# Optimization experiments

Hardware: AMD Instinct MI355X
Metric: run time of the kernel (lower is better)

## Reference

```python
import jax, jax.numpy as jnp
import numpy as np
import math

B, C, N = 8, 512, 2048

def setup_inputs() -> dict:
    key = jax.random.key(0)
    ks = jax.random.split(key, 7)
    s = 0.02
    return {
        "x": jax.random.normal(ks[0], (B, C, N), dtype=jnp.float32),
        "Wq": jax.random.normal(ks[1], (C // 2, C), dtype=jnp.float32) * s,
        "bq": jax.random.normal(ks[2], (C // 2,), dtype=jnp.float32) * s,
        "Wk": jax.random.normal(ks[3], (C // 2, C), dtype=jnp.float32) * s,
        "bk": jax.random.normal(ks[4], (C // 2,), dtype=jnp.float32) * s,
        "Wv": jax.random.normal(ks[5], (C, C), dtype=jnp.float32) * s,
        "bv": jax.random.normal(ks[6], (C,), dtype=jnp.float32) * s,
    }

def reference(x, Wq, bq, Wk, bk, Wv, bv):
    # pointwise conv1d == channel matmul: (O,C) x (B,C,N) -> (B,O,N)
    Q = jnp.einsum('oc,bcn->bon', Wq, x) + bq[None, :, None]  # (B, C/2, N)
    K = jnp.einsum('oc,bcn->bon', Wk, x) + bk[None, :, None]  # (B, C/2, N)
    V = jnp.einsum('oc,bcn->bon', Wv, x) + bv[None, :, None]  # (B, C, N)
    scale = 1.0 / math.sqrt(K.shape[1])
    A = jnp.einsum('bcn,bcm->bnm', Q, K) * scale              # (B, N, N)
    A = jax.nn.softmax(A, axis=-1)
    out = jnp.einsum('bcm,bnm->bcn', V, A)                    # V @ A^T
    return x + out
```

## Files before the change

### kernel.cpp

```cpp
#include <hip/hip_runtime.h>

#define B_ 8
#define C_ 512
#define N_ 2048
#define O_ 256

typedef unsigned short u16;
typedef unsigned char u8;
typedef unsigned int uint;
typedef float f32x4 __attribute__((ext_vector_type(4)));
typedef int i32x8 __attribute__((ext_vector_type(8)));

#define AS1 __attribute__((address_space(1)))
#define AS3 __attribute__((address_space(3)))

__device__ __forceinline__ u16 f2bf(float f) {
  union { float f; unsigned u; } v; v.f = f;
  return (u16)((v.u + 0x7fffu + ((v.u >> 16) & 1u)) >> 16);
}
__device__ __forceinline__ float bf2f(u16 h) {
  union { uint u; float f; } v; v.u = ((uint)h) << 16; return v.f;
}
__device__ __forceinline__ uint pk4_e4m3(float a, float b, float c, float d) {
  int r = __builtin_amdgcn_cvt_pk_fp8_f32(a, b, 0, false);
  r = __builtin_amdgcn_cvt_pk_fp8_f32(c, d, r, true);
  return (uint)r;
}

union MxFrag { i32x8 v; uint4 q[2]; };

__device__ __forceinline__ void mx_mainloop(
    const u8* __restrict__ Ag, int lda,
    const u8* __restrict__ Bg, int ldb, int K,
    u8 (&As)[128][128], u8 (&Bs)[128][128], f32x4 (&acc)[4][4])
{
  const int t = threadIdx.x;
  const int lane = t & 63;
  const int w = t >> 6;
  const int wm = (w >> 1) * 64, wn = (w & 1) * 64;
  const int lrow = lane & 15, quad = lane >> 4;
  const int swz = lrow & 7;
  const int r8 = lane >> 3;
  const int gsrc = (lane & 7) ^ r8;

  for (int k0 = 0; k0 < K; k0 += 128) {
#pragma unroll
    for (int i = 0; i < 4; i++) {
      int row = i * 32 + w * 8;
      __builtin_amdgcn_global_load_lds(
          (const AS1 uint*)(Ag + (size_t)(row + r8) * lda + k0 + gsrc * 16),
          (AS3 uint*)(&As[row][0]), 16, 0, 0);
      __builtin_amdgcn_global_load_lds(
          (const AS1 uint*)(Bg + (size_t)(row + r8) * ldb + k0 + gsrc * 16),
          (AS3 uint*)(&Bs[row][0]), 16, 0, 0);
    }
    __syncthreads();
    const int g0 = (quad * 2) ^ swz, g1 = (quad * 2 + 1) ^ swz;
    MxFrag af[4], bfr[4];
#pragma unroll
    for (int i = 0; i < 4; i++) {
      const u8* rp = &As[wm + i * 16 + lrow][0];
      af[i].q[0] = *(const uint4*)(rp + g0 * 16);
      af[i].q[1] = *(const uint4*)(rp + g1 * 16);
    }
#pragma unroll
    for (int j = 0; j < 4; j++) {
      const u8* rp = &Bs[wn + j * 16 + lrow][0];
      bfr[j].q[0] = *(const uint4*)(rp + g0 * 16);
      bfr[j].q[1] = *(const uint4*)(rp + g1 * 16);
    }
#pragma unroll
    for (int i = 0; i < 4; i++)
#pragma unroll
      for (int j = 0; j < 4; j++)
        acc[i][j] = __builtin_amdgcn_mfma_scale_f32_16x16x128_f8f6f4(
            af[i].v, bfr[j].v, acc[i][j],
            0, 0,
            0, 0x7f7f7f7f,
            0, 0x7f7f7f7f);
    __syncthreads();
  }
}

__device__ __forceinline__ void mx_mainloop_512(
    const u8* __restrict__ Ag, int lda,
    const u8* __restrict__ Bg, int ldb, int K,
    u8 (&As)[256][128], u8 (&Bs)[128][128], f32x4 (&acc)[4][4])
{
  const int t = threadIdx.x;
  const int lane = t & 63;
  const int w = t >> 6;
  const int wm = (w & 3) * 64, wn = (w >> 2) * 64;
  const int lrow = lane & 15, quad = lane >> 4;
  const int swz = lrow & 7;
  const int r8 = lane >> 3;
  const int gsrc = (lane & 7) ^ r8;

  for (int k0 = 0; k0 < K; k0 += 128) {
#pragma unroll
    for (int s = 0; s < 4; s++) {
      int row = (w * 4 + s) * 8;
      __builtin_amdgcn_global_load_lds(
          (const AS1 uint*)(Ag + (size_t)(row + r8) * lda + k0 + gsrc * 16),
          (AS3 uint*)(&As[row][0]), 16, 0, 0);
    }
#pragma unroll
    for (int s = 0; s < 2; s++) {
      int row = (w * 2 + s) * 8;
      __builtin_amdgcn_global_load_lds(
          (const AS1 uint*)(Bg + (size_t)(row + r8) * ldb + k0 + gsrc * 16),
          (AS3 uint*)(&Bs[row][0]), 16, 0, 0);
    }
    __syncthreads();
    const int g0 = (quad * 2) ^ swz, g1 = (quad * 2 + 1) ^ swz;
    MxFrag af[4], bfr[4];
#pragma unroll
    for (int i = 0; i < 4; i++) {
      const u8* rp = &As[wm + i * 16 + lrow][0];
      af[i].q[0] = *(const uint4*)(rp + g0 * 16);
      af[i].q[1] = *(const uint4*)(rp + g1 * 16);
    }
#pragma unroll
    for (int j = 0; j < 4; j++) {
      const u8* rp = &Bs[wn + j * 16 + lrow][0];
      bfr[j].q[0] = *(const uint4*)(rp + g0 * 16);
      bfr[j].q[1] = *(const uint4*)(rp + g1 * 16);
    }
#pragma unroll
    for (int i = 0; i < 4; i++)
#pragma unroll
      for (int j = 0; j < 4; j++)
        acc[i][j] = __builtin_amdgcn_mfma_scale_f32_16x16x128_f8f6f4(
            af[i].v, bfr[j].v, acc[i][j],
            0, 0, 0, 0x7f7f7f7f, 0, 0x7f7f7f7f);
    __syncthreads();
  }
}

__global__ __launch_bounds__(256) void prep_kernel(
    const float* __restrict__ x,
    const float* __restrict__ Wq, const float* __restrict__ Wk,
    const float* __restrict__ Wv,
    u8* __restrict__ xT8, u8* __restrict__ Wq8, u8* __restrict__ Wk8,
    u8* __restrict__ Wv8, float* __restrict__ rowsum)
{
  __shared__ u16 tile[64][72];
  const int bid = blockIdx.x;
  const int t = threadIdx.x;
  if (bid < 2048) {
    int b = bid >> 8;
    int n0 = (bid & 31) * 64;
    int c0 = ((bid >> 5) & 7) * 64;
    const float* src = x + (size_t)b * C_ * N_ + (size_t)c0 * N_ + n0;
    int r = t >> 4;
    int f4 = (t & 15) * 4;
#pragma unroll
    for (int i = 0; i < 4; i++) {
      int c = r + 16 * i;
      float4 v = *(const float4*)(src + (size_t)c * N_ + f4);
      tile[f4 + 0][c] = f2bf(v.x);
      tile[f4 + 1][c] = f2bf(v.y);
      tile[f4 + 2][c] = f2bf(v.z);
      tile[f4 + 3][c] = f2bf(v.w);
    }
    __syncthreads();
    u8* dst = xT8 + (size_t)b * N_ * C_ + (size_t)n0 * C_ + c0;
    int n = t >> 2;
    int cc = (t & 3) * 16;
    uint4 d;
    d.x = pk4_e4m3(bf2f(tile[n][cc + 0]), bf2f(tile[n][cc + 1]),
                   bf2f(tile[n][cc + 2]), bf2f(tile[n][cc + 3]));
    d.y = pk4_e4m3(bf2f(tile[n][cc + 4]), bf2f(tile[n][cc + 5]),
                   bf2f(tile[n][cc + 6]), bf2f(tile[n][cc + 7]));
    d.z = pk4_e4m3(bf2f(tile[n][cc + 8]), bf2f(tile[n][cc + 9]),
                   bf2f(tile[n][cc + 10]), bf2f(tile[n][cc + 11]));
    d.w = pk4_e4m3(bf2f(tile[n][cc + 12]), bf2f(tile[n][cc + 13]),
                   bf2f(tile[n][cc + 14]), bf2f(tile[n][cc + 15]));
    *(uint4*)(dst + (size_t)n * C_ + cc) = d;
  } else {
    int gid = (bid - 2048) * 256 + t;
    const float* src; u8* dst; int o;
    if (gid < 32768)      { src = Wq; dst = Wq8; o = gid; }
    else if (gid < 65536) { src = Wk; dst = Wk8; o = gid - 32768; }
    else                  { src = Wv; dst = Wv8; o = gid - 65536; }
    float4 v = *(const float4*)(src + (size_t)o * 4);
    *(uint*)(dst + (size_t)o * 4) = pk4_e4m3(v.x, v.y, v.z, v.w);
    if (gid < 4096) {
      float4 z = {0.f, 0.f, 0.f, 0.f};
      *(float4*)(rowsum + gid * 4) = z;
    }
  }
}

__global__ __launch_bounds__(256) void proj_all_kernel(
    const u8* __restrict__ xT8,
    const u8* __restrict__ Wq8, const float* __restrict__ bq,
    const u8* __restrict__ Wk8, const float* __restrict__ bk,
    const u8* __restrict__ Wv8, const float* __restrict__ bv,
    u8* __restrict__ Qt8, u8* __restrict__ Kt8, u8* __restrict__ V8)
{
  __shared__ __align__(16) u8 As[128][128], Bs[128][128];
  const int Lf = blockIdx.x +
                 (int)(gridDim.x * (blockIdx.y + gridDim.y * blockIdx.z));
  const int b = Lf & 7;
  const int rem = Lf >> 3;
  const int n0 = (rem & 15) * 128;
  const int sub = rem >> 4;
  const u8* xTb = xT8 + (size_t)b * N_ * C_ + (size_t)n0 * C_;

  const f32x4 zero = {0.f, 0.f, 0.f, 0.f};
  f32x4 acc[4][4];
#pragma unroll
  for (int i = 0; i < 4; i++)
#pragma unroll
    for (int j = 0; j < 4; j++) acc[i][j] = zero;

  const int lane = threadIdx.x & 63;
  const int w = threadIdx.x >> 6;
  const int wm = (w >> 1) * 64, wn = (w & 1) * 64;
  const int quad = lane >> 4, lcol = lane & 15;

  if (sub < 4) {
    const int isK = sub >> 1;
    const int o0 = (sub & 1) * 128;
    const u8* Wg = (isK ? Wk8 : Wq8) + (size_t)o0 * C_;
    const float* bias = isK ? bk : bq;
    u8* outp = (isK ? Kt8 : Qt8) + (size_t)b * N_ * O_;

    mx_mainloop(Wg, C_, xTb, C_, C_, As, Bs, acc);

#pragma unroll
    for (int i = 0; i < 4; i++) {
      int obase = o0 + wm + i * 16 + quad * 4;
      float4 bb = *(const float4*)(bias + obase);
#pragma unroll
      for (int j = 0; j < 4; j++) {
        int n = n0 + wn + j * 16 + lcol;
        uint d = pk4_e4m3(acc[i][j][0] + bb.x, acc[i][j][1] + bb.y,
                          acc[i][j][2] + bb.z, acc[i][j][3] + bb.w);
        *(uint*)(outp + (size_t)n * O_ + obase) = d;
      }
    }
  } else {
    const int c0 = (sub - 4) * 128;
    const u8* Wg = Wv8 + (size_t)c0 * C_;
    u8* outp = V8 + (size_t)b * C_ * N_;

    mx_mainloop(xTb, C_, Wg, C_, C_, As, Bs, acc);

#pragma unroll
    for (int j = 0; j < 4; j++) {
      int c = c0 + wn + j * 16 + lcol;
      float bb = bv[c];
#pragma unroll
      for (int i = 0; i < 4; i++) {
        int nbase = n0 + wm + i * 16 + quad * 4;
        uint d = pk4_e4m3(acc[i][j][0] + bb, acc[i][j][1] + bb,
                          acc[i][j][2] + bb, acc[i][j][3] + bb);
        *(uint*)(outp + (size_t)c * N_ + nbase) = d;
      }
    }
  }
}

__global__ __launch_bounds__(512) void attn_s_kernel(
    const u8* __restrict__ Qt8, const u8* __restrict__ Kt8,
    u8* __restrict__ P, float* __restrict__ rowsum)
{
  __shared__ __align__(16) u8 As[256][128], Bs[128][128];
  const int Lf = blockIdx.x +
                 (int)(gridDim.x * (blockIdx.y + gridDim.y * blockIdx.z));
  const int b = Lf & 7;
  const int rem = Lf >> 3;
  const int m0 = (rem & 7) * 256;
  const int n0 = (rem >> 3) * 128;
  const u8* Ag = Kt8 + (size_t)b * N_ * O_ + (size_t)m0 * O_;
  const u8* Bg = Qt8 + (size_t)b * N_ * O_ + (size_t)n0 * O_;

  const f32x4 zero = {0.f, 0.f, 0.f, 0.f};
  f32x4 acc[4][4];
#pragma unroll
  for (int i = 0; i < 4; i++)
#pragma unroll
    for (int j = 0; j < 4; j++) acc[i][j] = zero;

  mx_mainloop_512(Ag, O_, Bg, O_, O_, As, Bs, acc);

  u8* Pp = P + (size_t)b * N_ * N_;
  float* rs = rowsum + (size_t)b * N_;
  const int lane = threadIdx.x & 63;
  const int w = threadIdx.x >> 6;
  const int wm = (w & 3) * 64, wn = (w >> 2) * 64;
  const int quad = lane >> 4, lcol = lane & 15;

  float partial[4];
#pragma unroll
  for (int j = 0; j < 4; j++) partial[j] = 0.f;

#pragma unroll
  for (int j = 0; j < 4; j++) {
    int n = n0 + wn + j * 16 + lcol;
#pragma unroll
    for (int i = 0; i < 4; i++) {
      int mbase = m0 + wm + i * 16 + quad * 4;
      float p0 = __expf(acc[i][j][0] * 0.0625f);
      float p1 = __expf(acc[i][j][1] * 0.0625f);
      float p2 = __expf(acc[i][j][2] * 0.0625f);
      float p3 = __expf(acc[i][j][3] * 0.0625f);
      *(uint*)(Pp + (size_t)n * N_ + mbase) = pk4_e4m3(p0, p1, p2, p3);
      partial[j] += p0 + p1 + p2 + p3;
    }
  }
#pragma unroll
  for (int msk = 16; msk < 64; msk <<= 1)
#pragma unroll
    for (int j = 0; j < 4; j++)
      partial[j] += __shfl_xor(partial[j], msk);
  if (quad == 0) {
#pragma unroll
    for (int j = 0; j < 4; j++)
      atomicAdd(&rs[n0 + wn + j * 16 + lcol], partial[j]);
  }
}

__global__ __launch_bounds__(256) void attn_o_kernel(
    const u8* __restrict__ V, const u8* __restrict__ P,
    const float* __restrict__ rowsum, const float* __restrict__ x,
    float* __restrict__ out)
{
  __shared__ __align__(16) u8 As[128][128], Bs[128][128];
  const int Lf = blockIdx.x +
                 (int)(gridDim.x * (blockIdx.y + gridDim.y * blockIdx.z));
  const int b = Lf & 7;
  const int rem = Lf >> 3;
  const int c0 = (rem & 3) * 128;
  const int n0 = (rem >> 2) * 128;
  const u8* Ag = V + (size_t)b * C_ * N_ + (size_t)c0 * N_;
  const u8* Bg = P + (size_t)b * N_ * N_ + (size_t)n0 * N_;

  const f32x4 zero = {0.f, 0.f, 0.f, 0.f};
  f32x4 acc[4][4];
#pragma unroll
  for (int i = 0; i < 4; i++)
#pragma unroll
    for (int j = 0; j < 4; j++) acc[i][j] = zero;

  mx_mainloop(Ag, N_, Bg, N_, N_, As, Bs, acc);

  const int lane = threadIdx.x & 63;
  const int w = threadIdx.x >> 6;
  const int wm = (w >> 1) * 64, wn = (w & 1) * 64;
  const int quad = lane >> 4, lcol = lane & 15;

  const float* xb = x + (size_t)b * C_ * N_;
  float* ob = out + (size_t)b * C_ * N_;
  float invl[4];
#pragma unroll
  for (int j = 0; j < 4; j++)
    invl[j] = 1.f / rowsum[b * N_ + n0 + wn + j * 16 + lcol];

#pragma unroll
  for (int i = 0; i < 4; i++)
#pragma unroll
    for (int rr = 0; rr < 4; rr++) {
      int c = c0 + wm + i * 16 + quad * 4 + rr;
#pragma unroll
      for (int j = 0; j < 4; j++) {
        int n = n0 + wn + j * 16 + lcol;
        size_t idx = (size_t)c * N_ + n;
        ob[idx] = xb[idx] + acc[i][j][rr] * invl[j];
      }
    }
}

extern "C" void kernel_launch(void* const* d_in, const int* in_sizes, int n_in,
                              void* d_out, int out_size, void* d_ws, size_t ws_size,
                              hipStream_t stream)
{
  (void)in_sizes; (void)n_in; (void)out_size; (void)ws_size;
  const float* x  = (const float*)d_in[0];
  const float* Wq = (const float*)d_in[1];
  const float* bq = (const float*)d_in[2];
  const float* Wk = (const float*)d_in[3];
  const float* bk = (const float*)d_in[4];
  const float* Wv = (const float*)d_in[5];
  const float* bv = (const float*)d_in[6];
  float* out = (float*)d_out;

  char* ws = (char*)d_ws;
  size_t off = 0;
  auto carve = [&](size_t bytes) -> char* {
    char* p = ws + off;
    off += (bytes + 255) & ~(size_t)255;
    return p;
  };
  u8*  xT8  = (u8*) carve((size_t)B_ * N_ * C_);
  u8*  Wq8  = (u8*) carve((size_t)O_ * C_);
  u8*  Wk8  = (u8*) carve((size_t)O_ * C_);
  u8*  Wv8  = (u8*) carve((size_t)C_ * C_);
  u8*  Qt8  = (u8*) carve((size_t)B_ * N_ * O_);
  u8*  Kt8  = (u8*) carve((size_t)B_ * N_ * O_);
  u8*  Vb   = (u8*) carve((size_t)B_ * C_ * N_);
  u8*  P    = (u8*) carve((size_t)B_ * N_ * N_);
  float* rowsum = (float*)carve((size_t)B_ * N_ * 4);

  prep_kernel<<<dim3(2560), 256, 0, stream>>>(
      x, Wq, Wk, Wv, xT8, Wq8, Wk8, Wv8, rowsum);
  proj_all_kernel<<<dim3(16, 8, 8), 256, 0, stream>>>(
      xT8, Wq8, bq, Wk8, bk, Wv8, bv, Qt8, Kt8, Vb);
  attn_s_kernel<<<dim3(8, 16, 8), 512, 0, stream>>>(Qt8, Kt8, P, rowsum);
  attn_o_kernel<<<dim3(16, 4, 8), 256, 0, stream>>>(Vb, P, rowsum, x, out);
}
```

Baseline: 167.4 us.

## Shrink attn_s tiles to 128x128 and double K-step in attn_o mainloop

The score kernel now uses 128x128 tiles with 256 threads and reuses the generic mainloop, doubling its grid and dropping the 512-thread variant. The output kernel now loads two 128-wide K slabs per iteration into doubled LDS buffers, so it synchronises half as often per K. The aim is to cut barrier overhead in the P·V GEMM and to improve occupancy and balance in the score GEMM. The cost is more LDS per block in attn_o (64KB), which may lower occupancy, and more redundant K-operand loads in attn_s.

```diff
diff --git a/kernel.cpp b/kernel.cpp
--- a/kernel.cpp
+++ b/kernel.cpp
@@ -78,61 +78,6 @@
             0, 0,
             0, 0x7f7f7f7f,
             0, 0x7f7f7f7f);
-    __syncthreads();
-  }
-}
-
-__device__ __forceinline__ void mx_mainloop_512(
-    const u8* __restrict__ Ag, int lda,
-    const u8* __restrict__ Bg, int ldb, int K,
-    u8 (&As)[256][128], u8 (&Bs)[128][128], f32x4 (&acc)[4][4])
-{
-  const int t = threadIdx.x;
-  const int lane = t & 63;
-  const int w = t >> 6;
-  const int wm = (w & 3) * 64, wn = (w >> 2) * 64;
-  const int lrow = lane & 15, quad = lane >> 4;
-  const int swz = lrow & 7;
-  const int r8 = lane >> 3;
-  const int gsrc = (lane & 7) ^ r8;
-
-  for (int k0 = 0; k0 < K; k0 += 128) {
-#pragma unroll
-    for (int s = 0; s < 4; s++) {
-      int row = (w * 4 + s) * 8;
-      __builtin_amdgcn_global_load_lds(
-          (const AS1 uint*)(Ag + (size_t)(row + r8) * lda + k0 + gsrc * 16),
-          (AS3 uint*)(&As[row][0]), 16, 0, 0);
-    }
-#pragma unroll
-    for (int s = 0; s < 2; s++) {
-      int row = (w * 2 + s) * 8;
-      __builtin_amdgcn_global_load_lds(
-          (const AS1 uint*)(Bg + (size_t)(row + r8) * ldb + k0 + gsrc * 16),
-          (AS3 uint*)(&Bs[row][0]), 16, 0, 0);
-    }
-    __syncthreads();
-    const int g0 = (quad * 2) ^ swz, g1 = (quad * 2 + 1) ^ swz;
-    MxFrag af[4], bfr[4];
-#pragma unroll
-    for (int i = 0; i < 4; i++) {
-      const u8* rp = &As[wm + i * 16 + lrow][0];
-      af[i].q[0] = *(const uint4*)(rp + g0 * 16);
-      af[i].q[1] = *(const uint4*)(rp + g1 * 16);
-    }
-#pragma unroll
-    for (int j = 0; j < 4; j++) {
-      const u8* rp = &Bs[wn + j * 16 + lrow][0];
-      bfr[j].q[0] = *(const uint4*)(rp + g0 * 16);
-      bfr[j].q[1] = *(const uint4*)(rp + g1 * 16);
-    }
-#pragma unroll
-    for (int i = 0; i < 4; i++)
-#pragma unroll
-      for (int j = 0; j < 4; j++)
-        acc[i][j] = __builtin_amdgcn_mfma_scale_f32_16x16x128_f8f6f4(
-            af[i].v, bfr[j].v, acc[i][j],
-            0, 0, 0, 0x7f7f7f7f, 0, 0x7f7f7f7f);
     __syncthreads();
   }
 }
@@ -263,17 +208,17 @@
   }
 }
 
-__global__ __launch_bounds__(512) void attn_s_kernel(
+__global__ __launch_bounds__(256) void attn_s_kernel(
     const u8* __restrict__ Qt8, const u8* __restrict__ Kt8,
     u8* __restrict__ P, float* __restrict__ rowsum)
 {
-  __shared__ __align__(16) u8 As[256][128], Bs[128][128];
+  __shared__ __align__(16) u8 As[128][128], Bs[128][128];
   const int Lf = blockIdx.x +
                  (int)(gridDim.x * (blockIdx.y + gridDim.y * blockIdx.z));
   const int b = Lf & 7;
   const int rem = Lf >> 3;
-  const int m0 = (rem & 7) * 256;
-  const int n0 = (rem >> 3) * 128;
+  const int m0 = (rem & 15) * 128;
+  const int n0 = (rem >> 4) * 128;
   const u8* Ag = Kt8 + (size_t)b * N_ * O_ + (size_t)m0 * O_;
   const u8* Bg = Qt8 + (size_t)b * N_ * O_ + (size_t)n0 * O_;
 
@@ -284,13 +229,13 @@
 #pragma unroll
     for (int j = 0; j < 4; j++) acc[i][j] = zero;
 
-  mx_mainloop_512(Ag, O_, Bg, O_, O_, As, Bs, acc);
+  mx_mainloop(Ag, O_, Bg, O_, O_, As, Bs, acc);
 
   u8* Pp = P + (size_t)b * N_ * N_;
   float* rs = rowsum + (size_t)b * N_;
   const int lane = threadIdx.x & 63;
   const int w = threadIdx.x >> 6;
-  const int wm = (w & 3) * 64, wn = (w >> 2) * 64;
+  const int wm = (w >> 1) * 64, wn = (w & 1) * 64;
   const int quad = lane >> 4, lcol = lane & 15;
 
   float partial[4];
@@ -328,7 +273,7 @@
     const float* __restrict__ rowsum, const float* __restrict__ x,
     float* __restrict__ out)
 {
-  __shared__ __align__(16) u8 As[128][128], Bs[128][128];
+  __shared__ __align__(16) u8 As[2][128][128], Bs[2][128][128];
   const int Lf = blockIdx.x +
                  (int)(gridDim.x * (blockIdx.y + gridDim.y * blockIdx.z));
   const int b = Lf & 7;
@@ -338,6 +283,15 @@
   const u8* Ag = V + (size_t)b * C_ * N_ + (size_t)c0 * N_;
   const u8* Bg = P + (size_t)b * N_ * N_ + (size_t)n0 * N_;
 
+  const int t = threadIdx.x;
+  const int lane = t & 63;
+  const int w = t >> 6;
+  const int wm = (w >> 1) * 64, wn = (w & 1) * 64;
+  const int lrow = lane & 15, quad = lane >> 4;
+  const int swz = lrow & 7;
+  const int r8 = lane >> 3;
+  const int gsrc = (lane & 7) ^ r8;
+
   const f32x4 zero = {0.f, 0.f, 0.f, 0.f};
   f32x4 acc[4][4];
 #pragma unroll
@@ -345,13 +299,50 @@
 #pragma unroll
     for (int j = 0; j < 4; j++) acc[i][j] = zero;
 
-  mx_mainloop(Ag, N_, Bg, N_, N_, As, Bs, acc);
-
-  const int lane = threadIdx.x & 63;
-  const int w = threadIdx.x >> 6;
-  const int wm = (w >> 1) * 64, wn = (w & 1) * 64;
-  const int quad = lane >> 4, lcol = lane & 15;
-
+  for (int k0 = 0; k0 < N_; k0 += 256) {
+#pragma unroll
+    for (int hb = 0; hb < 2; hb++) {
+      const int kk = k0 + hb * 128;
+#pragma unroll
+      for (int i = 0; i < 4; i++) {
+        int row = i * 32 + w * 8;
+        __builtin_amdgcn_global_load_lds(
+            (const AS1 uint*)(Ag + (size_t)(row + r8) * N_ + kk + gsrc * 16),
+            (AS3 uint*)(&As[hb][row][0]), 16, 0, 0);
+        __builtin_amdgcn_global_load_lds(
+            (const AS1 uint*)(Bg + (size_t)(row + r8) * N_ + kk + gsrc * 16),
+            (AS3 uint*)(&Bs[hb][row][0]), 16, 0, 0);
+      }
+    }
+    __syncthreads();
+    const int g0 = (quad * 2) ^ swz, g1 = (quad * 2 + 1) ^ swz;
+#pragma unroll
+    for (int hb = 0; hb < 2; hb++) {
+      MxFrag af[4], bfr[4];
+#pragma unroll
+      for (int i = 0; i < 4; i++) {
+        const u8* rp = &As[hb][wm + i * 16 + lrow][0];
+        af[i].q[0] = *(const uint4*)(rp + g0 * 16);
+        af[i].q[1] = *(const uint4*)(rp + g1 * 16);
+      }
+#pragma unroll
+      for (int j = 0; j < 4; j++) {
+        const u8* rp = &Bs[hb][wn + j * 16 + lrow][0];
+        bfr[j].q[0] = *(const uint4*)(rp + g0 * 16);
+        bfr[j].q[1] = *(const uint4*)(rp + g1 * 16);
+      }
+#pragma unroll
+      for (int i = 0; i < 4; i++)
+#pragma unroll
+        for (int j = 0; j < 4; j++)
+          acc[i][j] = __builtin_amdgcn_mfma_scale_f32_16x16x128_f8f6f4(
+              af[i].v, bfr[j].v, acc[i][j],
+              0, 0, 0, 0x7f7f7f7f, 0, 0x7f7f7f7f);
+    }
+    __syncthreads();
+  }
+
+  const int lcol = lane & 15;
   const float* xb = x + (size_t)b * C_ * N_;
   float* ob = out + (size_t)b * C_ * N_;
   float invl[4];
@@ -408,6 +399,6 @@
       x, Wq, Wk, Wv, xT8, Wq8, Wk8, Wv8, rowsum);
   proj_all_kernel<<<dim3(16, 8, 8), 256, 0, stream>>>(
       xT8, Wq8, bq, Wk8, bk, Wv8, bv, Qt8, Kt8, Vb);
-  attn_s_kernel<<<dim3(8, 16, 8), 512, 0, stream>>>(Qt8, Kt8, P, rowsum);
+  attn_s_kernel<<<dim3(16, 16, 8), 256, 0, stream>>>(Qt8, Kt8, P, rowsum);
   attn_o_kernel<<<dim3(16, 4, 8), 256, 0, stream>>>(Vb, P, rowsum, x, out);
 }
```

New measurement: 161.2 us. -3.7%, faster.
